# Kernel optimization log

Measured on AMD Instinct MI355X. Metric: run time of the kernel, lower is better.

## Reference

```python
import jax, jax.numpy as jnp
import numpy as np

STRIDE = 1  # conv stride from __init__


def setup_inputs() -> dict:
    key = jax.random.key(0)
    k1, k2, k3 = jax.random.split(key, 3)
    prot1 = jax.random.normal(k1, (4, 1024, 8, 64), dtype=jnp.float32)
    prot2 = jax.random.normal(k2, (4, 1024, 8, 64), dtype=jnp.float32)
    # W: (no_filters, no_channels, no_dims, window_size)
    W = jax.random.normal(k3, (32, 8, 64, 7), dtype=jnp.float32)
    return {"prot1": prot1, "prot2": prot2, "W": W}


def _project(x, W, stride):
    """Fused equivalent of unfold + broadcast-mul + sum over (C, window).

    x: (N, H, C, D), W: (F, C, D, w) -> (N, F, H', D) with H' = (H - w)//stride + 1.
    This is a grouped 1D conv: D groups, each mixing C input channels into F outputs.
    """
    N, H, C, D = x.shape
    Fn, _, _, w = W.shape
    xg = jnp.transpose(x, (0, 3, 2, 1)).reshape(N, D * C, H)        # (N, D*C, H)
    Wg = jnp.transpose(W, (2, 0, 1, 3)).reshape(D * Fn, C, w)       # (D*F, C, w)
    out = jax.lax.conv_general_dilated(
        xg, Wg, window_strides=(stride,), padding='VALID',
        dimension_numbers=('NCH', 'OIH', 'NCH'), feature_group_count=D)
    Hp = out.shape[-1]
    return jnp.transpose(out.reshape(N, D, Fn, Hp), (0, 2, 3, 1))   # (N, F, H', D)


def reference(prot1, prot2, W):
    q1 = _project(prot1, W, STRIDE)   # (N, F, H1', D)
    q2 = _project(prot2, W, STRIDE)   # (N, F, H2', D)
    H1p, H2p = q1.shape[2], q2.shape[2]
    scale = jnp.sqrt(jnp.asarray(H1p * H2p, dtype=q1.dtype))
    att = jnp.einsum('nfhd,nfgd->nfhg', q1, q2) / scale             # (N, F, H1', H2')
    a = jax.nn.softmax(att, axis=3)
    p1 = jnp.einsum('nfhg,nfgd->nfhd', a, q2)                       # (N, F, H1', D)
    # NB: source does transpose(att, 2, 2) (a no-op) and multiplies the SAME
    # softmax matrix by the UPDATED p1folds; we reproduce that faithfully.
    p2 = jnp.einsum('nfhg,nfgd->nfhd', a, p1)                       # (N, F, H1', D)
    out1 = jnp.tanh(jnp.transpose(p1, (0, 2, 1, 3)))                # (N, H1', F, D)
    out2 = jnp.tanh(jnp.transpose(p2, (0, 2, 1, 3)))
    # Dropout is identity in eval mode (and dropout_p=0.0 here).
    return (out1, out2)
```

## Files before the change

kernel.cpp:

```cpp
#include <hip/hip_runtime.h>
#include <math.h>

typedef __bf16 bf16_t;
typedef bf16_t bf16x4 __attribute__((ext_vector_type(4)));
typedef bf16_t bf16x8 __attribute__((ext_vector_type(8)));
typedef float  f32x16 __attribute__((ext_vector_type(16)));

#define HH 1024
#define CC 8
#define DD 64
#define FF 32
#define WW 7
#define HP 1018
#define HPAD 1024
#define NF 128
#define QOUT (NF*HP*DD)
#define QWS ((size_t)NF*HPAD*DD)

#if __has_builtin(__builtin_amdgcn_exp2f)
#define EXP2(x) __builtin_amdgcn_exp2f(x)
#else
#define EXP2(x) __expf((x) * 0.6931471805599453f)
#endif

#define QSCALE (1.442695040888963f / 1018.f)

__device__ __forceinline__ int vaddr(int row, int col) {
    return row*64 + ((((col>>3) ^ (row&7) ^ ((row>>2)&7)))<<3) + (col&7);
}

__global__ __launch_bounds__(256) void wprep_kernel(
    const float* __restrict__ Wt, float* __restrict__ Wp)
{
    const int idx = blockIdx.x * 256 + threadIdx.x;
    if (idx < FF*CC*DD*WW) {
        const int j = idx % WW;
        int t = idx / WW;
        const int d = t % DD; t /= DD;
        const int c = t % CC;
        const int f = t / CC;
        Wp[((f*CC + c)*WW + j)*DD + d] = Wt[idx];
    }
}

__global__ __launch_bounds__(256) void conv_kernel(
    const float* __restrict__ x1, const float* __restrict__ x2,
    const float* __restrict__ Wp, bf16_t* __restrict__ q1, bf16_t* __restrict__ q2)
{
    __shared__ float xs[38*512];
    const int zin = blockIdx.z & 1;
    const int fh = blockIdx.z >> 1;
    const float* x = zin ? x2 : x1;
    bf16_t* q = zin ? q2 : q1;
    const float qs = zin ? 1.f : QSCALE;
    const int n = blockIdx.y;
    const int hb = blockIdx.x * 32;
    const int tid = threadIdx.x;

    const float4* xg = (const float4*)(x + (size_t)n*HH*512);
    for (int i = tid; i < 38*128; i += 256) {
        const int row = hb + (i >> 7);
        float4 v = {0.f, 0.f, 0.f, 0.f};
        if (row < HH) v = xg[(size_t)row*128 + (i & 127)];
        const int r = i >> 7;
        const int c = (i & 127) >> 4;
        const int d0 = ((i & 127) & 15) * 4;
        xs[r*512 + (d0+0)*8 + c] = v.x;
        xs[r*512 + (d0+1)*8 + c] = v.y;
        xs[r*512 + (d0+2)*8 + c] = v.z;
        xs[r*512 + (d0+3)*8 + c] = v.w;
    }
    __syncthreads();

    const int d = tid & 63;
    const int fq = tid >> 6;
    for (int fi = 0; fi < 4; ++fi) {
        const int f = fq*8 + fh*4 + fi;
        float w[CC][WW];
#pragma unroll
        for (int c = 0; c < CC; ++c)
#pragma unroll
            for (int j = 0; j < WW; ++j)
                w[c][j] = Wp[((f*CC + c)*WW + j)*DD + d];
#pragma unroll
        for (int hc = 0; hc < 2; ++hc) {
            float acc[16];
#pragma unroll
            for (int i = 0; i < 16; ++i) acc[i] = 0.f;
#pragma unroll
            for (int rr = 0; rr < 22; ++rr) {
                const float4 a = *(const float4*)&xs[(hc*16 + rr)*512 + d*8 + 0];
                const float4 b = *(const float4*)&xs[(hc*16 + rr)*512 + d*8 + 4];
                const float xv[8] = {a.x, a.y, a.z, a.w, b.x, b.y, b.z, b.w};
#pragma unroll
                for (int j = 0; j < WW; ++j) {
                    const int i = rr - j;
                    if (i >= 0 && i < 16) {
#pragma unroll
                        for (int c = 0; c < CC; ++c)
                            acc[i] = fmaf(xv[c], w[c][j], acc[i]);
                    }
                }
            }
#pragma unroll
            for (int i = 0; i < 16; ++i) {
                const int h = hb + hc*16 + i;
                const float v = (h < HP) ? acc[i]*qs : 0.f;
                q[((size_t)(n*FF + f)*HPAD + h)*DD + d] = (bf16_t)v;
            }
        }
    }
}

__device__ __forceinline__ float fast_tanh(float x) {
    const float t = __expf(2.f * x);
    return (t - 1.f) / (t + 1.f);
}

template<int MODE>
__global__ __launch_bounds__(256, 2) void flash(
    const bf16_t* __restrict__ q1, const bf16_t* __restrict__ q2,
    const bf16_t* __restrict__ vsrc, bf16_t* __restrict__ p1out,
    float* __restrict__ out)
{
    __shared__ __align__(16) bf16_t Vt[2][64*64];

    const int head = blockIdx.y;
    const int n = head >> 5, f = head & 31;
    const int tid = threadIdx.x;
    const int w = tid >> 6;
    const int lane = tid & 63;
    const int lid = lane & 31;
    const int half = lane >> 5;
    const int hb = blockIdx.x * 256 + w * 64;

    const size_t qoff = (size_t)head * HPAD * DD;
    const int vswz = (lid & 7) ^ (lid >> 2);

    const int gq = tid >> 4;
    const int dq = tid & 15;
    const int cgb = 4*((gq>>1)&1) + 8*(gq&1) + 16*(gq>>2);

    const bf16_t* vptr = (MODE == 1) ? vsrc : q2;

    const bf16_t* bp = q1 + qoff + (size_t)(hb + lid)*DD + 8*half;
    const bf16_t* ap = q2 + qoff + (size_t)lid*DD + 8*half;
    const bf16_t* vp = vptr + qoff + (size_t)(4*gq)*DD + 4*dq;

    bf16x8 bq1[2][4];
#pragma unroll
    for (int nt = 0; nt < 2; ++nt)
#pragma unroll
        for (int kt = 0; kt < 4; ++kt)
            bq1[nt][kt] = *(const bf16x8*)&bp[(size_t)(32*nt)*DD + 16*kt];

    bf16x8 aq[2][4];
#pragma unroll
    for (int mt = 0; mt < 2; ++mt)
#pragma unroll
        for (int kt = 0; kt < 4; ++kt)
            aq[mt][kt] = *(const bf16x8*)&ap[(size_t)(32*mt)*DD + 16*kt];

    bf16x4 rV[4];
#pragma unroll
    for (int i = 0; i < 4; ++i)
        rV[i] = *(const bf16x4*)&vp[(size_t)i*DD];
#pragma unroll
    for (int j = 0; j < 4; ++j) {
        bf16x4 c = { rV[0][j], rV[1][j], rV[2][j], rV[3][j] };
        *(bf16x4*)&Vt[0][vaddr(4*dq + j, cgb)] = c;
    }
#pragma unroll
    for (int i = 0; i < 4; ++i)
        rV[i] = *(const bf16x4*)&vp[(size_t)(64 + i)*DD];

    f32x16 O[2][2] = {};
    float lacc[2] = {0.f, 0.f};

    __syncthreads();

    for (int t = 0; t < 16; ++t) {
        const int g0 = t << 6;
        const bf16_t* vtc = Vt[t & 1];

        if (t + 1 < 16) {
            bf16_t* vtn = Vt[(t + 1) & 1];
#pragma unroll
            for (int j = 0; j < 4; ++j) {
                bf16x4 c = { rV[0][j], rV[1][j], rV[2][j], rV[3][j] };
                *(bf16x4*)&vtn[vaddr(4*dq + j, cgb)] = c;
            }
            if (t + 2 < 16) {
#pragma unroll
                for (int i = 0; i < 4; ++i)
                    rV[i] = *(const bf16x4*)&vp[(size_t)((t + 2)*64 + i)*DD];
            }
        }

        const bool tail = (g0 + 64 > HP);

#pragma unroll
        for (int mt = 0; mt < 2; ++mt) {
            f32x16 C[2] = {};
            __builtin_amdgcn_s_setprio(1);
#pragma unroll
            for (int kt = 0; kt < 4; ++kt) {
                C[0] = __builtin_amdgcn_mfma_f32_32x32x16_bf16(aq[mt][kt], bq1[0][kt], C[0], 0,0,0);
                C[1] = __builtin_amdgcn_mfma_f32_32x32x16_bf16(aq[mt][kt], bq1[1][kt], C[1], 0,0,0);
            }
            __builtin_amdgcn_s_setprio(0);
            if (g0 + 64 < HPAD) {
#pragma unroll
                for (int kt = 0; kt < 4; ++kt)
                    aq[mt][kt] = *(const bf16x8*)&ap[(size_t)(g0 + 64 + 32*mt)*DD + 16*kt];
            }
            bf16x8 af[2][2];
#pragma unroll
            for (int nt = 0; nt < 2; ++nt) {
                float ls = 0.f;
#pragma unroll
                for (int s = 0; s < 16; ++s) {
                    float e = EXP2(C[nt][s]);
                    if (tail) {
                        const int gg = g0 + 32*mt + (s&3) + 8*(s>>2) + 4*half;
                        if (gg >= HP) e = 0.f;
                    }
                    ls += e;
                    af[nt][s>>3][s&7] = (bf16_t)e;
                }
                lacc[nt] += ls;
            }
            __builtin_amdgcn_s_setprio(1);
#pragma unroll
            for (int u = 0; u < 2; ++u) {
#pragma unroll
                for (int dt = 0; dt < 2; ++dt) {
                    const int chunk = (4*mt + 2*u + half) ^ vswz;
                    bf16x8 b = *(const bf16x8*)&vtc[(32*dt + lid)*64 + chunk*8];
                    O[0][dt] = __builtin_amdgcn_mfma_f32_32x32x16_bf16(af[0][u], b, O[0][dt], 0,0,0);
                    O[1][dt] = __builtin_amdgcn_mfma_f32_32x32x16_bf16(af[1][u], b, O[1][dt], 0,0,0);
                }
            }
            __builtin_amdgcn_s_setprio(0);
        }
        __syncthreads();
    }

    float linv[2];
#pragma unroll
    for (int nt = 0; nt < 2; ++nt) {
        const float l = lacc[nt] + __shfl_xor(lacc[nt], 32);
        linv[nt] = 1.f / l;
    }
#pragma unroll
    for (int ht = 0; ht < 2; ++ht) {
#pragma unroll
        for (int s = 0; s < 16; ++s) {
            const int R = (s&3) + 8*(s>>2) + 4*half;
            const float li = __shfl(linv[ht], R);
            const int hg = hb + 32*ht + R;
#pragma unroll
            for (int dt = 0; dt < 2; ++dt) {
                const int d = 32*dt + lid;
                const float val = O[ht][dt][s] * li;
                if (hg < HP)
                    out[(((size_t)n*HP + hg)*FF + f)*DD + d] = fast_tanh(val);
                if (MODE == 0)
                    p1out[qoff + (size_t)hg*DD + d] = (bf16_t)(hg < HP ? val : 0.f);
            }
        }
    }
}

extern "C" void kernel_launch(void* const* d_in, const int* in_sizes, int n_in,
                              void* d_out, int out_size, void* d_ws, size_t ws_size,
                              hipStream_t stream)
{
    const float* prot1 = (const float*)d_in[0];
    const float* prot2 = (const float*)d_in[1];
    const float* Wt    = (const float*)d_in[2];
    float* out = (float*)d_out;

    bf16_t* q1b = (bf16_t*)d_ws;
    bf16_t* q2b = q1b + QWS;
    bf16_t* p1b = q2b + QWS;
    float* Wp   = (float*)(p1b + QWS);

    wprep_kernel<<<dim3(448), 256, 0, stream>>>(Wt, Wp);
    conv_kernel<<<dim3(32, 4, 4), 256, 0, stream>>>(prot1, prot2, Wp, q1b, q2b);
    flash<0><<<dim3(4, NF), 256, 0, stream>>>(q1b, q2b, q2b, p1b, out);
    flash<1><<<dim3(4, NF), 256, 0, stream>>>(q1b, q2b, p1b, p1b, out + QOUT);
}
```

Measured before the change: 222.6 us.

## Restructure conv kernel: natural smem layout, two filters per pass, doubled grid

The input tile is now copied into shared memory in its native (row, c, d) order as float4 stores instead of being scattered into a transposed d-major layout. Each thread keeps weights for two filters in registers and accumulates both from the same shared-memory reads, so each loaded input value feeds twice as many FMAs. Each block now handles two filters instead of four, and the grid's z dimension doubles to cover all filters, giving more blocks. The cost is a larger register footprint (two weight sets and two accumulator arrays) and scalar shared loads in place of float4 loads.

```diff
diff --git a/kernel.cpp b/kernel.cpp
--- a/kernel.cpp
+++ b/kernel.cpp
@@ -58,54 +58,63 @@
     const int tid = threadIdx.x;
 
     const float4* xg = (const float4*)(x + (size_t)n*HH*512);
+    float4* xsv = (float4*)xs;
     for (int i = tid; i < 38*128; i += 256) {
         const int row = hb + (i >> 7);
         float4 v = {0.f, 0.f, 0.f, 0.f};
         if (row < HH) v = xg[(size_t)row*128 + (i & 127)];
-        const int r = i >> 7;
-        const int c = (i & 127) >> 4;
-        const int d0 = ((i & 127) & 15) * 4;
-        xs[r*512 + (d0+0)*8 + c] = v.x;
-        xs[r*512 + (d0+1)*8 + c] = v.y;
-        xs[r*512 + (d0+2)*8 + c] = v.z;
-        xs[r*512 + (d0+3)*8 + c] = v.w;
+        xsv[i] = v;
     }
     __syncthreads();
 
     const int d = tid & 63;
     const int fq = tid >> 6;
-    for (int fi = 0; fi < 4; ++fi) {
-        const int f = fq*8 + fh*4 + fi;
-        float w[CC][WW];
+
+    float w[2][CC][WW];
+#pragma unroll
+    for (int fi = 0; fi < 2; ++fi) {
+        const int f = fq*8 + fh*2 + fi;
 #pragma unroll
         for (int c = 0; c < CC; ++c)
 #pragma unroll
             for (int j = 0; j < WW; ++j)
-                w[c][j] = Wp[((f*CC + c)*WW + j)*DD + d];
-#pragma unroll
-        for (int hc = 0; hc < 2; ++hc) {
-            float acc[16];
-#pragma unroll
-            for (int i = 0; i < 16; ++i) acc[i] = 0.f;
-#pragma unroll
-            for (int rr = 0; rr < 22; ++rr) {
-                const float4 a = *(const float4*)&xs[(hc*16 + rr)*512 + d*8 + 0];
-                const float4 b = *(const float4*)&xs[(hc*16 + rr)*512 + d*8 + 4];
-                const float xv[8] = {a.x, a.y, a.z, a.w, b.x, b.y, b.z, b.w};
+                w[fi][c][j] = Wp[((f*CC + c)*WW + j)*DD + d];
+    }
+
+#pragma unroll
+    for (int hc = 0; hc < 2; ++hc) {
+        float acc[2][16];
+#pragma unroll
+        for (int fi = 0; fi < 2; ++fi)
+#pragma unroll
+            for (int i = 0; i < 16; ++i) acc[fi][i] = 0.f;
+
+#pragma unroll
+        for (int rr = 0; rr < 22; ++rr) {
+            float xv[CC];
+#pragma unroll
+            for (int c = 0; c < CC; ++c)
+                xv[c] = xs[(hc*16 + rr)*512 + c*64 + d];
+#pragma unroll
+            for (int fi = 0; fi < 2; ++fi)
 #pragma unroll
                 for (int j = 0; j < WW; ++j) {
                     const int i = rr - j;
                     if (i >= 0 && i < 16) {
 #pragma unroll
                         for (int c = 0; c < CC; ++c)
-                            acc[i] = fmaf(xv[c], w[c][j], acc[i]);
+                            acc[fi][i] = fmaf(xv[c], w[fi][c][j], acc[fi][i]);
                     }
                 }
-            }
+        }
+
+#pragma unroll
+        for (int fi = 0; fi < 2; ++fi) {
+            const int f = fq*8 + fh*2 + fi;
 #pragma unroll
             for (int i = 0; i < 16; ++i) {
                 const int h = hb + hc*16 + i;
-                const float v = (h < HP) ? acc[i]*qs : 0.f;
+                const float v = (h < HP) ? acc[fi][i]*qs : 0.f;
                 q[((size_t)(n*FF + f)*HPAD + h)*DD + d] = (bf16_t)v;
             }
         }
@@ -287,7 +296,7 @@
     float* Wp   = (float*)(p1b + QWS);
 
     wprep_kernel<<<dim3(448), 256, 0, stream>>>(Wt, Wp);
-    conv_kernel<<<dim3(32, 4, 4), 256, 0, stream>>>(prot1, prot2, Wp, q1b, q2b);
+    conv_kernel<<<dim3(32, 4, 8), 256, 0, stream>>>(prot1, prot2, Wp, q1b, q2b);
     flash<0><<<dim3(4, NF), 256, 0, stream>>>(q1b, q2b, q2b, p1b, out);
     flash<1><<<dim3(4, NF), 256, 0, stream>>>(q1b, q2b, p1b, p1b, out + QOUT);
 }
```

Measured after the change: 212.0 us. 1.05x faster.
